# Performance work log

Measured on AMD Instinct MI355X. Metric: run time of the kernel, lower is better.

Reference implementation:

```python
import jax, jax.numpy as jnp
import numpy as np

M_STEP = 3  # model_args.m_step
E_STEP = 3  # model_args.e_step


def setup_inputs() -> dict:
    key = jax.random.key(0)
    ks = jax.random.split(key, 8)
    B, N, F = 1024, 11, 512   # batch, num_nodes (=round_id+2), message_size
    H = 512                   # link_hidden_size
    sc = 1.0 / np.sqrt(F)
    rnd = lambda k, shape: (jax.random.normal(k, shape, jnp.float32) * sc)
    return {
        "node_features": jax.random.normal(ks[0], (B, N, F), jnp.float32),
        "W1": rnd(ks[1], (H, F)),
        "b1": jnp.zeros((H,), jnp.float32),
        "W2": rnd(ks[2], (H, H)),
        "b2": jnp.zeros((H,), jnp.float32),
        "w_out": rnd(ks[3], (H,)),
        "b_out": jnp.zeros((), jnp.float32),
        "W_ih": rnd(ks[4], (3 * F, F)),  # GRU input weights (r,z,n), bias=False
        "W_hh": rnd(ks[5], (3 * F, F)),  # GRU hidden weights
    }


def _link_adj(x, W1, b1, W2, b2, w_out, b_out):
    # LinkFunction('graphconvattn'): pairwise node-feature interactions -> 1x1 conv stack -> [B,N,N]
    # x: [B,F,N]
    e = x[:, :, :, None] * x[:, :, None, :]                                  # [B,F,N,N]
    h = jax.nn.relu(jnp.einsum('bfij,gf->bgij', e, W1) + b1[None, :, None, None])
    h = jax.nn.relu(jnp.einsum('bfij,gf->bgij', h, W2) + b2[None, :, None, None])
    return jnp.einsum('bfij,f->bij', h, w_out) + b_out                       # [B,N,N]


def _gru_cell(m, h, W_ih, W_hh):
    # torch nn.GRU cell, bias=False, gate order (r, z, n)
    gi = m @ W_ih.T
    gh = h @ W_hh.T
    ir, iz, inn = jnp.split(gi, 3, axis=-1)
    hr, hz, hn = jnp.split(gh, 3, axis=-1)
    r = jax.nn.sigmoid(ir + hr)
    z = jax.nn.sigmoid(iz + hz)
    n = jnp.tanh(inn + r * hn)
    return (1.0 - z) * n + z * h


def reference(node_features, W1, b1, W2, b2, w_out, b_out, W_ih, W_hh):
    x0 = jnp.transpose(node_features, (0, 2, 1))   # [B,F,N]
    N = x0.shape[2]
    zidx = N - 1                                   # only the question node is updated
    col = x0[:, :, zidx]
    adj = None
    for t in range(M_STEP):
        # pred_node_feats[t]: original features with node z replaced by latest estimate
        pred = x0.at[:, :, zidx].set(col)
        adj = _link_adj(pred, W1, b1, W2, b2, w_out, b_out)
        A = jax.nn.softmax(adj, axis=2)            # softmax over neighbors
        a_z = A[:, zidx, :]                        # [B,N]
        h = pred
        for s in range(E_STEP):
            m_z = jnp.einsum('bj,bfj->bf', a_z, h)             # weighted message
            h_z = _gru_cell(m_z, h[:, :, zidx], W_ih, W_hh)    # GRU update
            h = h.at[:, :, zidx].set(h_z)
        col = h[:, :, zidx]
    # returns (pred_adj_mat from last m-step, final feature of node z)
    return adj, col
```

## Files before the change

kernel.cpp:

```cpp
#include <hip/hip_runtime.h>
#include <hip/hip_bf16.h>
#include <math.h>

#define Bsz 1024
#define Nn  11
#define Ff  512
#define Zi  10
#define G3  1536

#define PEC 65

typedef __attribute__((ext_vector_type(8))) short bfrag;
typedef __attribute__((ext_vector_type(4))) float f32x4;

__device__ __forceinline__ unsigned f2bf(float f) {
    __hip_bfloat16 h = __float2bfloat16(f);
    return (unsigned)*reinterpret_cast<unsigned short*>(&h);
}
__device__ __forceinline__ uint4 pack8(float v0, float v1, float v2, float v3,
                                       float v4, float v5, float v6, float v7) {
    uint4 pk;
    pk.x = f2bf(v0) | (f2bf(v1) << 16);
    pk.y = f2bf(v2) | (f2bf(v3) << 16);
    pk.z = f2bf(v4) | (f2bf(v5) << 16);
    pk.w = f2bf(v6) | (f2bf(v7) << 16);
    return pk;
}
__device__ __forceinline__ void pair_decode(int mode, int p, int& pi, int& pj) {
    if (mode == 0) { int r = p, i = 0; while (r >= Nn - i) { r -= Nn - i; ++i; } pi = i; pj = i + r; }
    else { pi = p; pj = Zi; }
}
__device__ __forceinline__ void gl_lds16(const void* src, void* dst) {
    __builtin_amdgcn_global_load_lds((const __attribute__((address_space(1))) void*)src,
                                     (__attribute__((address_space(3))) void*)dst, 16, 0, 0);
}

__global__ void init_col_kernel(const float* __restrict__ nf, float* __restrict__ col) {
    int idx = blockIdx.x * 256 + threadIdx.x;
    int b = idx >> 9, f = idx & 511;
    col[idx] = nf[(b * Nn + Zi) * Ff + f];
}

__global__ void pack_w_kernel(const float* __restrict__ src,
                              unsigned short* __restrict__ dst, int lgBW) {
    int idx = blockIdx.x * 256 + threadIdx.x;
    int g = idx >> 6, kq = idx & 63;
    int nb = g >> lgBW, gl = g & ((1 << lgBW) - 1);
    const float* s = src + g * Ff + kq * 8;
    float4 a = *(const float4*)s, b = *(const float4*)(s + 4);
    uint4 pk = pack8(a.x, a.y, a.z, a.w, b.x, b.y, b.z, b.w);
    long long dc = (((long long)(nb << 6) + kq) << lgBW) + gl;
    *(uint4*)((char*)dst + dc * 16) = pk;
}

__global__ __launch_bounds__(512, 2) void link_kernel(
    const float* __restrict__ nf, const float* __restrict__ colp,
    const unsigned short* __restrict__ W1p, const float* __restrict__ b1,
    const unsigned short* __restrict__ W2p, const float* __restrict__ b2,
    const float* __restrict__ w_out, const float* __restrict__ b_out,
    float* __restrict__ adj, int mode)
{
    __shared__ __align__(16) char Eb[64 * PEC * 16];
    __shared__ float Pl[8][64];

    const int tid = threadIdx.x;
    const int pr  = blockIdx.x >> 4;
    const int bc  = blockIdx.x & 15;
    int pi, pj; pair_decode(mode, pr, pi, pj);

    const int wid  = tid >> 6;
    const int l    = tid & 63;
    const int lr16 = l & 15;
    const int kq4  = l >> 4;

    const bfrag* W1c = (const bfrag*)W1p;
    const bfrag* W2c = (const bfrag*)W2p;
    const int wcb = wid * 64 + lr16;

    bfrag wb0[4], wb1[4];
    auto loadW = [&](int gs, bfrag* dst) {
        const bfrag* Wc = (gs >= 16) ? W2c : W1c;
        const int base = ((gs & 15) * 4 + kq4) * 512 + wcb;
#pragma unroll
        for (int nt = 0; nt < 4; ++nt) dst[nt] = Wc[base + nt * 16];
    };

    loadW(0, wb0);

    {
        const int row = tid >> 3;
        const int kc  = tid & 7;
        const int b   = bc * 64 + row;
        const float* xi = (pi == Zi) ? (colp + b * Ff) : (nf + (b * Nn + pi) * Ff);
        const float* xj = (pj == Zi) ? (colp + b * Ff) : (nf + (b * Nn + pj) * Ff);
#pragma unroll
        for (int i = 0; i < 8; ++i) {
            const int k0 = kc * 64 + i * 8;
            const int plane = k0 >> 3;
            float4 u0 = *(const float4*)(xi + k0), u1 = *(const float4*)(xi + k0 + 4);
            float4 v0 = *(const float4*)(xj + k0), v1 = *(const float4*)(xj + k0 + 4);
            *(uint4*)(&Eb[(plane * PEC + row) * 16]) =
                pack8(u0.x*v0.x, u0.y*v0.y, u0.z*v0.z, u0.w*v0.w,
                      u1.x*v1.x, u1.y*v1.y, u1.z*v1.z, u1.w*v1.w);
        }
    }
    __syncthreads();

    f32x4 acc[4][4];
#pragma unroll
    for (int mt = 0; mt < 4; ++mt)
#pragma unroll
        for (int nt = 0; nt < 4; ++nt) acc[mt][nt] = (f32x4){0.f, 0.f, 0.f, 0.f};

#define DO_STEP(S, WB) { \
    const int ebase = ((S) & 15) * 4 + kq4; \
    bfrag a0 = *(const bfrag*)(&Eb[(ebase * PEC +      lr16) * 16]); \
    bfrag a1 = *(const bfrag*)(&Eb[(ebase * PEC + 16 + lr16) * 16]); \
    bfrag a2 = *(const bfrag*)(&Eb[(ebase * PEC + 32 + lr16) * 16]); \
    bfrag a3 = *(const bfrag*)(&Eb[(ebase * PEC + 48 + lr16) * 16]); \
    acc[0][0] = __builtin_amdgcn_mfma_f32_16x16x32_bf16(a0, WB[0], acc[0][0], 0, 0, 0); \
    acc[0][1] = __builtin_amdgcn_mfma_f32_16x16x32_bf16(a0, WB[1], acc[0][1], 0, 0, 0); \
    acc[0][2] = __builtin_amdgcn_mfma_f32_16x16x32_bf16(a0, WB[2], acc[0][2], 0, 0, 0); \
    acc[0][3] = __builtin_amdgcn_mfma_f32_16x16x32_bf16(a0, WB[3], acc[0][3], 0, 0, 0); \
    acc[1][0] = __builtin_amdgcn_mfma_f32_16x16x32_bf16(a1, WB[0], acc[1][0], 0, 0, 0); \
    acc[1][1] = __builtin_amdgcn_mfma_f32_16x16x32_bf16(a1, WB[1], acc[1][1], 0, 0, 0); \
    acc[1][2] = __builtin_amdgcn_mfma_f32_16x16x32_bf16(a1, WB[2], acc[1][2], 0, 0, 0); \
    acc[1][3] = __builtin_amdgcn_mfma_f32_16x16x32_bf16(a1, WB[3], acc[1][3], 0, 0, 0); \
    acc[2][0] = __builtin_amdgcn_mfma_f32_16x16x32_bf16(a2, WB[0], acc[2][0], 0, 0, 0); \
    acc[2][1] = __builtin_amdgcn_mfma_f32_16x16x32_bf16(a2, WB[1], acc[2][1], 0, 0, 0); \
    acc[2][2] = __builtin_amdgcn_mfma_f32_16x16x32_bf16(a2, WB[2], acc[2][2], 0, 0, 0); \
    acc[2][3] = __builtin_amdgcn_mfma_f32_16x16x32_bf16(a2, WB[3], acc[2][3], 0, 0, 0); \
    acc[3][0] = __builtin_amdgcn_mfma_f32_16x16x32_bf16(a3, WB[0], acc[3][0], 0, 0, 0); \
    acc[3][1] = __builtin_amdgcn_mfma_f32_16x16x32_bf16(a3, WB[1], acc[3][1], 0, 0, 0); \
    acc[3][2] = __builtin_amdgcn_mfma_f32_16x16x32_bf16(a3, WB[2], acc[3][2], 0, 0, 0); \
    acc[3][3] = __builtin_amdgcn_mfma_f32_16x16x32_bf16(a3, WB[3], acc[3][3], 0, 0, 0); }

#pragma unroll 1
    for (int s2 = 0; s2 < 8; ++s2) {
        const int s = 2 * s2;
        loadW(s + 1, wb1);
        DO_STEP(s, wb0)
        loadW(s + 2, wb0);
        DO_STEP(s + 1, wb1)
    }

    __syncthreads();
    {
#pragma unroll
        for (int nt = 0; nt < 4; ++nt) {
            const int c  = wid * 64 + nt * 16 + lr16;
            const float bv = b1[c];
#pragma unroll
            for (int mt = 0; mt < 4; ++mt)
#pragma unroll
                for (int reg = 0; reg < 4; ++reg) {
                    int row = mt * 16 + kq4 * 4 + reg;
                    float v = fmaxf(acc[mt][nt][reg] + bv, 0.f);
                    *(unsigned short*)(&Eb[((c >> 3) * PEC + row) * 16 + (c & 7) * 2]) =
                        (unsigned short)f2bf(v);
                }
        }
#pragma unroll
        for (int mt = 0; mt < 4; ++mt)
#pragma unroll
            for (int nt = 0; nt < 4; ++nt) acc[mt][nt] = (f32x4){0.f, 0.f, 0.f, 0.f};
    }
    __syncthreads();

#pragma unroll 1
    for (int s2 = 0; s2 < 8; ++s2) {
        const int s = 16 + 2 * s2;
        loadW(s + 1, wb1);
        DO_STEP(s, wb0)
        if (s2 < 7) loadW(s + 2, wb0);
        DO_STEP(s + 1, wb1)
    }
#undef DO_STEP

    {
        float rs[4][4];
#pragma unroll
        for (int mt = 0; mt < 4; ++mt)
#pragma unroll
            for (int reg = 0; reg < 4; ++reg) rs[mt][reg] = 0.f;
#pragma unroll
        for (int nt = 0; nt < 4; ++nt) {
            const int c  = wid * 64 + nt * 16 + lr16;
            const float bv = b2[c];
            const float wv = w_out[c];
#pragma unroll
            for (int mt = 0; mt < 4; ++mt)
#pragma unroll
                for (int reg = 0; reg < 4; ++reg)
                    rs[mt][reg] += fmaxf(acc[mt][nt][reg] + bv, 0.f) * wv;
        }
#pragma unroll
        for (int off = 1; off < 16; off <<= 1)
#pragma unroll
            for (int mt = 0; mt < 4; ++mt)
#pragma unroll
                for (int reg = 0; reg < 4; ++reg)
                    rs[mt][reg] += __shfl_xor(rs[mt][reg], off);
        if (lr16 == 0) {
#pragma unroll
            for (int mt = 0; mt < 4; ++mt)
#pragma unroll
                for (int reg = 0; reg < 4; ++reg) {
                    int row = mt * 16 + kq4 * 4 + reg;
                    Pl[wid][row] = rs[mt][reg];
                }
        }
    }
    __syncthreads();
    if (tid < 64) {
        float v = b_out[0];
#pragma unroll
        for (int w = 0; w < 8; ++w) v += Pl[w][tid];
        int b = bc * 64 + tid;
        adj[b * (Nn * Nn) + pi * Nn + pj] = v;
        if (pi != pj) adj[b * (Nn * Nn) + pj * Nn + pi] = v;
    }
}

__global__ void softmax_az_kernel(const float* __restrict__ adj, float* __restrict__ a_z) {
    int b = blockIdx.x * 256 + threadIdx.x;
    if (b >= Bsz) return;
    const float* row = adj + b * (Nn * Nn) + Zi * Nn;
    float mx = row[0];
#pragma unroll
    for (int j = 1; j < Nn; ++j) mx = fmaxf(mx, row[j]);
    float e[Nn]; float s = 0.f;
#pragma unroll
    for (int j = 0; j < Nn; ++j) { e[j] = expf(row[j] - mx); s += e[j]; }
    float inv = 1.f / s;
#pragma unroll
    for (int j = 0; j < Nn; ++j) a_z[b * Nn + j] = e[j] * inv;
}

__global__ void mzpack_kernel(const float* __restrict__ nf, const float* __restrict__ a_z,
                              const float* __restrict__ col,
                              unsigned short* __restrict__ m_zp,
                              unsigned short* __restrict__ colbf) {
    int idx = blockIdx.x * 256 + threadIdx.x;
    int b = idx >> 6, kq = idx & 63;
    const float* az = a_z + b * Nn;
    const int f0 = kq * 8;
    float4 c0 = *(const float4*)(col + b * Ff + f0);
    float4 c1 = *(const float4*)(col + b * Ff + f0 + 4);
    float az10 = az[Zi];
    float s0 = az10 * c0.x, s1 = az10 * c0.y, s2 = az10 * c0.z, s3 = az10 * c0.w;
    float s4 = az10 * c1.x, s5 = az10 * c1.y, s6 = az10 * c1.z, s7 = az10 * c1.w;
#pragma unroll
    for (int j = 0; j < Nn - 1; ++j) {
        float aj = az[j];
        const float* p = nf + (b * Nn + j) * Ff + f0;
        float4 n0 = *(const float4*)p, n1 = *(const float4*)(p + 4);
        s0 += aj * n0.x; s1 += aj * n0.y; s2 += aj * n0.z; s3 += aj * n0.w;
        s4 += aj * n1.x; s5 += aj * n1.y; s6 += aj * n1.z; s7 += aj * n1.w;
    }
    long long dc = (((long long)(b >> 6) * 64 + kq) << 6) + (b & 63);
    *(uint4*)((char*)m_zp + dc * 16)  = pack8(s0, s1, s2, s3, s4, s5, s6, s7);
    *(uint4*)((char*)colbf + dc * 16) = pack8(c0.x, c0.y, c0.z, c0.w, c1.x, c1.y, c1.z, c1.w);
}

__global__ __launch_bounds__(256, 2) void gates_kernel(
    const unsigned short* __restrict__ m_zp, const unsigned short* __restrict__ colbf,
    const unsigned short* __restrict__ Wihp, const unsigned short* __restrict__ Whhp,
    float* __restrict__ gi, float* __restrict__ gh)
{
    __shared__ __align__(16) char Ab[64 * 64 * 16];

    const int xb = blockIdx.x, bc = blockIdx.y, tid = threadIdx.x;
    const bool isGi = xb < 6;
    const int nbase = (isGi ? xb : xb - 6) * 256;
    const unsigned short* Ap = isGi ? m_zp : colbf;
    const unsigned short* Wp = isGi ? Wihp : Whhp;
    float* C = isGi ? gi : gh;

    const int wid  = tid >> 6;
    const int l    = tid & 63;
    const int lr16 = l & 15;
    const int kq4  = l >> 4;

    const bfrag* Wc = (const bfrag*)Wp;
    const int wcb = ((nbase >> 9) << 15) + (nbase & 511) + wid * 64 + lr16;

    bfrag wb0[4], wb1[4];
    auto loadW = [&](int s, bfrag* dst) {
        const int base = wcb + (s * 4 + kq4) * 512;
#pragma unroll
        for (int nt = 0; nt < 4; ++nt) dst[nt] = Wc[base + nt * 16];
    };

    loadW(0, wb0);

#pragma unroll
    for (int i = 0; i < 16; ++i) {
        int cb = i * 256 + wid * 64;
        gl_lds16(Ap + ((long long)bc * 4096 + cb + l) * 8, (char*)Ab + cb * 16);
    }
    __syncthreads();

    f32x4 acc[4][4];
#pragma unroll
    for (int mt = 0; mt < 4; ++mt)
#pragma unroll
        for (int nt = 0; nt < 4; ++nt) acc[mt][nt] = (f32x4){0.f, 0.f, 0.f, 0.f};

#define DO_STEPG(S, WB) { \
    const int ebase = (S) * 4 + kq4; \
    bfrag a0 = *(const bfrag*)(&Ab[(ebase * 64 +      lr16) * 16]); \
    bfrag a1 = *(const bfrag*)(&Ab[(ebase * 64 + 16 + lr16) * 16]); \
    bfrag a2 = *(const bfrag*)(&Ab[(ebase * 64 + 32 + lr16) * 16]); \
    bfrag a3 = *(const bfrag*)(&Ab[(ebase * 64 + 48 + lr16) * 16]); \
    acc[0][0] = __builtin_amdgcn_mfma_f32_16x16x32_bf16(a0, WB[0], acc[0][0], 0, 0, 0); \
    acc[0][1] = __builtin_amdgcn_mfma_f32_16x16x32_bf16(a0, WB[1], acc[0][1], 0, 0, 0); \
    acc[0][2] = __builtin_amdgcn_mfma_f32_16x16x32_bf16(a0, WB[2], acc[0][2], 0, 0, 0); \
    acc[0][3] = __builtin_amdgcn_mfma_f32_16x16x32_bf16(a0, WB[3], acc[0][3], 0, 0, 0); \
    acc[1][0] = __builtin_amdgcn_mfma_f32_16x16x32_bf16(a1, WB[0], acc[1][0], 0, 0, 0); \
    acc[1][1] = __builtin_amdgcn_mfma_f32_16x16x32_bf16(a1, WB[1], acc[1][1], 0, 0, 0); \
    acc[1][2] = __builtin_amdgcn_mfma_f32_16x16x32_bf16(a1, WB[2], acc[1][2], 0, 0, 0); \
    acc[1][3] = __builtin_amdgcn_mfma_f32_16x16x32_bf16(a1, WB[3], acc[1][3], 0, 0, 0); \
    acc[2][0] = __builtin_amdgcn_mfma_f32_16x16x32_bf16(a2, WB[0], acc[2][0], 0, 0, 0); \
    acc[2][1] = __builtin_amdgcn_mfma_f32_16x16x32_bf16(a2, WB[1], acc[2][1], 0, 0, 0); \
    acc[2][2] = __builtin_amdgcn_mfma_f32_16x16x32_bf16(a2, WB[2], acc[2][2], 0, 0, 0); \
    acc[2][3] = __builtin_amdgcn_mfma_f32_16x16x32_bf16(a2, WB[3], acc[2][3], 0, 0, 0); \
    acc[3][0] = __builtin_amdgcn_mfma_f32_16x16x32_bf16(a3, WB[0], acc[3][0], 0, 0, 0); \
    acc[3][1] = __builtin_amdgcn_mfma_f32_16x16x32_bf16(a3, WB[1], acc[3][1], 0, 0, 0); \
    acc[3][2] = __builtin_amdgcn_mfma_f32_16x16x32_bf16(a3, WB[2], acc[3][2], 0, 0, 0); \
    acc[3][3] = __builtin_amdgcn_mfma_f32_16x16x32_bf16(a3, WB[3], acc[3][3], 0, 0, 0); }

#pragma unroll 1
    for (int s2 = 0; s2 < 8; ++s2) {
        const int s = 2 * s2;
        loadW(s + 1, wb1);
        DO_STEPG(s, wb0)
        if (s2 < 7) loadW(s + 2, wb0);
        DO_STEPG(s + 1, wb1)
    }
#undef DO_STEPG

#pragma unroll
    for (int nt = 0; nt < 4; ++nt) {
        const int c = nbase + wid * 64 + nt * 16 + lr16;
#pragma unroll
        for (int mt = 0; mt < 4; ++mt)
#pragma unroll
            for (int reg = 0; reg < 4; ++reg) {
                int row = mt * 16 + kq4 * 4 + reg;
                C[(bc * 64 + row) * G3 + c] = acc[mt][nt][reg];
            }
    }
}

__global__ void gru_kernel(const float* __restrict__ gi, const float* __restrict__ gh,
                           float* __restrict__ col) {
    int idx = blockIdx.x * 256 + threadIdx.x;
    int b = idx >> 7, f = (idx & 127) * 4;
    const float* gib = gi + b * G3;
    const float* ghb = gh + b * G3;
    float4 ir = *(const float4*)(gib + f);
    float4 iz = *(const float4*)(gib + Ff + f);
    float4 in = *(const float4*)(gib + 2 * Ff + f);
    float4 hr = *(const float4*)(ghb + f);
    float4 hz = *(const float4*)(ghb + Ff + f);
    float4 hn = *(const float4*)(ghb + 2 * Ff + f);
    float4 h  = *(const float4*)(col + b * Ff + f);
    float4 o;
#define GRU1(c) { \
    float r = 1.f / (1.f + expf(-(ir.c + hr.c))); \
    float z = 1.f / (1.f + expf(-(iz.c + hz.c))); \
    float n = tanhf(in.c + r * hn.c); \
    o.c = (1.f - z) * n + z * h.c; }
    GRU1(x) GRU1(y) GRU1(z) GRU1(w)
#undef GRU1
    *(float4*)(col + b * Ff + f) = o;
}

extern "C" void kernel_launch(void* const* d_in, const int* in_sizes, int n_in,
                              void* d_out, int out_size, void* d_ws, size_t ws_size,
                              hipStream_t stream) {
    const float* nf    = (const float*)d_in[0];
    const float* W1    = (const float*)d_in[1];
    const float* b1    = (const float*)d_in[2];
    const float* W2    = (const float*)d_in[3];
    const float* b2    = (const float*)d_in[4];
    const float* w_out = (const float*)d_in[5];
    const float* b_out = (const float*)d_in[6];
    const float* W_ih  = (const float*)d_in[7];
    const float* W_hh  = (const float*)d_in[8];

    float* adj = (float*)d_out;
    float* col = adj + Bsz * Nn * Nn;

    unsigned short* W1p   = (unsigned short*)d_ws;
    unsigned short* W2p   = W1p + Ff * Ff;
    unsigned short* Wihp  = W2p + Ff * Ff;
    unsigned short* Whhp  = Wihp + G3 * Ff;
    float* a_z            = (float*)(Whhp + G3 * Ff);
    unsigned short* m_zp  = (unsigned short*)(a_z + 16384);
    unsigned short* colbf = m_zp + Bsz * Ff;
    float* gi             = (float*)(colbf + Bsz * Ff);
    float* gh             = gi + Bsz * G3;

    init_col_kernel<<<(Bsz * Ff) / 256, 256, 0, stream>>>(nf, col);
    pack_w_kernel<<<(Ff * 64) / 256, 256, 0, stream>>>(W1, W1p, 9);
    pack_w_kernel<<<(Ff * 64) / 256, 256, 0, stream>>>(W2, W2p, 9);
    pack_w_kernel<<<(G3 * 64) / 256, 256, 0, stream>>>(W_ih, Wihp, 9);
    pack_w_kernel<<<(G3 * 64) / 256, 256, 0, stream>>>(W_hh, Whhp, 9);

    for (int t = 0; t < 3; ++t) {
        const int mode   = (t == 0) ? 0 : 1;
        const int npairs = (t == 0) ? 66 : 11;

        link_kernel<<<npairs * 16, 512, 0, stream>>>(nf, col, W1p, b1, W2p, b2,
                                                     w_out, b_out, adj, mode);
        softmax_az_kernel<<<Bsz / 256, 256, 0, stream>>>(adj, a_z);

        for (int s = 0; s < 3; ++s) {
            mzpack_kernel<<<(Bsz * 64) / 256, 256, 0, stream>>>(nf, a_z, col, m_zp, colbf);
            gates_kernel<<<dim3(12, 16), 256, 0, stream>>>(m_zp, colbf, Wihp, Whhp, gi, gh);
            gru_kernel<<<(Bsz * Ff) / 4 / 256, 256, 0, stream>>>(gi, gh, col);
        }
    }
}
```

Measured before the change: 364.4 us.

## Hoist fixed neighbor message sum out of e-steps and fuse packing into GRU

The weighted sum over the ten fixed neighbor nodes is computed once per m-step into m_fix instead of being recomputed every e-step. The GRU kernel now also writes the bf16-packed hidden state and the next message (m_fix + a_z10*h), so the separate mzpack launch per e-step disappears. This cuts repeated reads of node_features and one launch per e-step, at the cost of an extra fp32 buffer, two extra kernels per m-step, and a redundant message write on the last e-step. A clamp is also added to the weight prefetch index in gates_kernel.

```diff
diff --git a/kernel.cpp b/kernel.cpp
--- a/kernel.cpp
+++ b/kernel.cpp
@@ -35,10 +35,16 @@
                                      (__attribute__((address_space(3))) void*)dst, 16, 0, 0);
 }
 
-__global__ void init_col_kernel(const float* __restrict__ nf, float* __restrict__ col) {
+__global__ void init_col2_kernel(const float* __restrict__ nf, float* __restrict__ col,
+                                 unsigned short* __restrict__ colbf) {
     int idx = blockIdx.x * 256 + threadIdx.x;
-    int b = idx >> 9, f = idx & 511;
-    col[idx] = nf[(b * Nn + Zi) * Ff + f];
+    int b = idx >> 6, kq = idx & 63;
+    const float* s = nf + (b * Nn + Zi) * Ff + kq * 8;
+    float4 a = *(const float4*)s, c = *(const float4*)(s + 4);
+    *(float4*)(col + b * Ff + kq * 8)     = a;
+    *(float4*)(col + b * Ff + kq * 8 + 4) = c;
+    long long dc = (((long long)(b >> 6) * 64 + kq) << 6) + (b & 63);
+    *(uint4*)((char*)colbf + dc * 16) = pack8(a.x, a.y, a.z, a.w, c.x, c.y, c.z, c.w);
 }
 
 __global__ void pack_w_kernel(const float* __restrict__ src,
@@ -237,19 +243,13 @@
     for (int j = 0; j < Nn; ++j) a_z[b * Nn + j] = e[j] * inv;
 }
 
-__global__ void mzpack_kernel(const float* __restrict__ nf, const float* __restrict__ a_z,
-                              const float* __restrict__ col,
-                              unsigned short* __restrict__ m_zp,
-                              unsigned short* __restrict__ colbf) {
+__global__ void mfix_kernel(const float* __restrict__ nf, const float* __restrict__ a_z,
+                            float* __restrict__ m_fix) {
     int idx = blockIdx.x * 256 + threadIdx.x;
     int b = idx >> 6, kq = idx & 63;
     const float* az = a_z + b * Nn;
     const int f0 = kq * 8;
-    float4 c0 = *(const float4*)(col + b * Ff + f0);
-    float4 c1 = *(const float4*)(col + b * Ff + f0 + 4);
-    float az10 = az[Zi];
-    float s0 = az10 * c0.x, s1 = az10 * c0.y, s2 = az10 * c0.z, s3 = az10 * c0.w;
-    float s4 = az10 * c1.x, s5 = az10 * c1.y, s6 = az10 * c1.z, s7 = az10 * c1.w;
+    float s0 = 0.f, s1 = 0.f, s2 = 0.f, s3 = 0.f, s4 = 0.f, s5 = 0.f, s6 = 0.f, s7 = 0.f;
 #pragma unroll
     for (int j = 0; j < Nn - 1; ++j) {
         float aj = az[j];
@@ -258,9 +258,25 @@
         s0 += aj * n0.x; s1 += aj * n0.y; s2 += aj * n0.z; s3 += aj * n0.w;
         s4 += aj * n1.x; s5 += aj * n1.y; s6 += aj * n1.z; s7 += aj * n1.w;
     }
+    *(float4*)(m_fix + b * Ff + f0)     = (float4){s0, s1, s2, s3};
+    *(float4*)(m_fix + b * Ff + f0 + 4) = (float4){s4, s5, s6, s7};
+}
+
+__global__ void mzinit_kernel(const float* __restrict__ m_fix, const float* __restrict__ a_z,
+                              const float* __restrict__ col,
+                              unsigned short* __restrict__ m_zp) {
+    int idx = blockIdx.x * 256 + threadIdx.x;
+    int b = idx >> 6, kq = idx & 63;
+    const int f0 = kq * 8;
+    const float az10 = a_z[b * Nn + Zi];
+    float4 m0 = *(const float4*)(m_fix + b * Ff + f0);
+    float4 m1 = *(const float4*)(m_fix + b * Ff + f0 + 4);
+    float4 c0 = *(const float4*)(col + b * Ff + f0);
+    float4 c1 = *(const float4*)(col + b * Ff + f0 + 4);
     long long dc = (((long long)(b >> 6) * 64 + kq) << 6) + (b & 63);
-    *(uint4*)((char*)m_zp + dc * 16)  = pack8(s0, s1, s2, s3, s4, s5, s6, s7);
-    *(uint4*)((char*)colbf + dc * 16) = pack8(c0.x, c0.y, c0.z, c0.w, c1.x, c1.y, c1.z, c1.w);
+    *(uint4*)((char*)m_zp + dc * 16) =
+        pack8(m0.x + az10*c0.x, m0.y + az10*c0.y, m0.z + az10*c0.z, m0.w + az10*c0.w,
+              m1.x + az10*c1.x, m1.y + az10*c1.y, m1.z + az10*c1.z, m1.w + az10*c1.w);
 }
 
 __global__ __launch_bounds__(256, 2) void gates_kernel(
@@ -287,6 +303,7 @@
 
     bfrag wb0[4], wb1[4];
     auto loadW = [&](int s, bfrag* dst) {
+        if (s > 15) s = 15;
         const int base = wcb + (s * 4 + kq4) * 512;
 #pragma unroll
         for (int nt = 0; nt < 4; ++nt) dst[nt] = Wc[base + nt * 16];
@@ -353,28 +370,52 @@
     }
 }
 
-__global__ void gru_kernel(const float* __restrict__ gi, const float* __restrict__ gh,
-                           float* __restrict__ col) {
+__global__ void gru3_kernel(const float* __restrict__ gi, const float* __restrict__ gh,
+                            const float* __restrict__ m_fix, const float* __restrict__ a_z,
+                            float* __restrict__ col,
+                            unsigned short* __restrict__ colbf,
+                            unsigned short* __restrict__ m_zp) {
     int idx = blockIdx.x * 256 + threadIdx.x;
-    int b = idx >> 7, f = (idx & 127) * 4;
-    const float* gib = gi + b * G3;
-    const float* ghb = gh + b * G3;
-    float4 ir = *(const float4*)(gib + f);
-    float4 iz = *(const float4*)(gib + Ff + f);
-    float4 in = *(const float4*)(gib + 2 * Ff + f);
-    float4 hr = *(const float4*)(ghb + f);
-    float4 hz = *(const float4*)(ghb + Ff + f);
-    float4 hn = *(const float4*)(ghb + 2 * Ff + f);
-    float4 h  = *(const float4*)(col + b * Ff + f);
-    float4 o;
-#define GRU1(c) { \
-    float r = 1.f / (1.f + expf(-(ir.c + hr.c))); \
-    float z = 1.f / (1.f + expf(-(iz.c + hz.c))); \
-    float n = tanhf(in.c + r * hn.c); \
-    o.c = (1.f - z) * n + z * h.c; }
-    GRU1(x) GRU1(y) GRU1(z) GRU1(w)
-#undef GRU1
-    *(float4*)(col + b * Ff + f) = o;
+    int b = idx >> 6, kq = idx & 63;
+    const int f0 = kq * 8;
+    const float* gib = gi + (long long)b * G3;
+    const float* ghb = gh + (long long)b * G3;
+    float4 ir0 = *(const float4*)(gib + f0),        ir1 = *(const float4*)(gib + f0 + 4);
+    float4 iz0 = *(const float4*)(gib + 512 + f0),  iz1 = *(const float4*)(gib + 512 + f0 + 4);
+    float4 in0 = *(const float4*)(gib + 1024 + f0), in1 = *(const float4*)(gib + 1024 + f0 + 4);
+    float4 hr0 = *(const float4*)(ghb + f0),        hr1 = *(const float4*)(ghb + f0 + 4);
+    float4 hz0 = *(const float4*)(ghb + 512 + f0),  hz1 = *(const float4*)(ghb + 512 + f0 + 4);
+    float4 hn0 = *(const float4*)(ghb + 1024 + f0), hn1 = *(const float4*)(ghb + 1024 + f0 + 4);
+    float4 h0  = *(const float4*)(col + b * Ff + f0);
+    float4 h1  = *(const float4*)(col + b * Ff + f0 + 4);
+
+    float o[8];
+#define GRUC(K, IR, IZ, IN, HR, HZ, HN, H) { \
+    float r = 1.f / (1.f + expf(-((IR) + (HR)))); \
+    float z = 1.f / (1.f + expf(-((IZ) + (HZ)))); \
+    float n = tanhf((IN) + r * (HN)); \
+    o[K] = (1.f - z) * n + z * (H); }
+    GRUC(0, ir0.x, iz0.x, in0.x, hr0.x, hz0.x, hn0.x, h0.x)
+    GRUC(1, ir0.y, iz0.y, in0.y, hr0.y, hz0.y, hn0.y, h0.y)
+    GRUC(2, ir0.z, iz0.z, in0.z, hr0.z, hz0.z, hn0.z, h0.z)
+    GRUC(3, ir0.w, iz0.w, in0.w, hr0.w, hz0.w, hn0.w, h0.w)
+    GRUC(4, ir1.x, iz1.x, in1.x, hr1.x, hz1.x, hn1.x, h1.x)
+    GRUC(5, ir1.y, iz1.y, in1.y, hr1.y, hz1.y, hn1.y, h1.y)
+    GRUC(6, ir1.z, iz1.z, in1.z, hr1.z, hz1.z, hn1.z, h1.z)
+    GRUC(7, ir1.w, iz1.w, in1.w, hr1.w, hz1.w, hn1.w, h1.w)
+#undef GRUC
+
+    *(float4*)(col + b * Ff + f0)     = (float4){o[0], o[1], o[2], o[3]};
+    *(float4*)(col + b * Ff + f0 + 4) = (float4){o[4], o[5], o[6], o[7]};
+    long long dc = (((long long)(b >> 6) * 64 + kq) << 6) + (b & 63);
+    *(uint4*)((char*)colbf + dc * 16) = pack8(o[0], o[1], o[2], o[3], o[4], o[5], o[6], o[7]);
+
+    const float az10 = a_z[b * Nn + Zi];
+    float4 m0 = *(const float4*)(m_fix + b * Ff + f0);
+    float4 m1 = *(const float4*)(m_fix + b * Ff + f0 + 4);
+    *(uint4*)((char*)m_zp + dc * 16) =
+        pack8(m0.x + az10*o[0], m0.y + az10*o[1], m0.z + az10*o[2], m0.w + az10*o[3],
+              m1.x + az10*o[4], m1.y + az10*o[5], m1.z + az10*o[6], m1.w + az10*o[7]);
 }
 
 extern "C" void kernel_launch(void* const* d_in, const int* in_sizes, int n_in,
@@ -398,12 +439,13 @@
     unsigned short* Wihp  = W2p + Ff * Ff;
     unsigned short* Whhp  = Wihp + G3 * Ff;
     float* a_z            = (float*)(Whhp + G3 * Ff);
-    unsigned short* m_zp  = (unsigned short*)(a_z + 16384);
+    float* m_fix          = a_z + 16384;
+    unsigned short* m_zp  = (unsigned short*)(m_fix + Bsz * Ff);
     unsigned short* colbf = m_zp + Bsz * Ff;
     float* gi             = (float*)(colbf + Bsz * Ff);
     float* gh             = gi + Bsz * G3;
 
-    init_col_kernel<<<(Bsz * Ff) / 256, 256, 0, stream>>>(nf, col);
+    init_col2_kernel<<<(Bsz * 64) / 256, 256, 0, stream>>>(nf, col, colbf);
     pack_w_kernel<<<(Ff * 64) / 256, 256, 0, stream>>>(W1, W1p, 9);
     pack_w_kernel<<<(Ff * 64) / 256, 256, 0, stream>>>(W2, W2p, 9);
     pack_w_kernel<<<(G3 * 64) / 256, 256, 0, stream>>>(W_ih, Wihp, 9);
@@ -416,11 +458,13 @@
         link_kernel<<<npairs * 16, 512, 0, stream>>>(nf, col, W1p, b1, W2p, b2,
                                                      w_out, b_out, adj, mode);
         softmax_az_kernel<<<Bsz / 256, 256, 0, stream>>>(adj, a_z);
+        mfix_kernel<<<(Bsz * 64) / 256, 256, 0, stream>>>(nf, a_z, m_fix);
+        mzinit_kernel<<<(Bsz * 64) / 256, 256, 0, stream>>>(m_fix, a_z, col, m_zp);
 
         for (int s = 0; s < 3; ++s) {
-            mzpack_kernel<<<(Bsz * 64) / 256, 256, 0, stream>>>(nf, a_z, col, m_zp, colbf);
             gates_kernel<<<dim3(12, 16), 256, 0, stream>>>(m_zp, colbf, Wihp, Whhp, gi, gh);
-            gru_kernel<<<(Bsz * Ff) / 4 / 256, 256, 0, stream>>>(gi, gh, col);
+            gru3_kernel<<<(Bsz * 64) / 256, 256, 0, stream>>>(gi, gh, m_fix, a_z,
+                                                              col, colbf, m_zp);
         }
     }
 }
```

New measurement: 366.1 us. About the same (+0.5%).
